# Kernel optimization log

Hardware: AMD Instinct MI355X
Metric: run time of the kernel (lower is better)

The kernel has to match this reference:

```python
import jax, jax.numpy as jnp
import numpy as np

E, D, H, K, DIL, T = 8, 768, 3072, 3, 1, 16384


def _conv1d(x, w, b, dilation):
    # x: [1, C_in, L]; w: [C_out, C_in, K]; torch Conv1d with SAME padding
    pad = dilation * (w.shape[-1] - 1) // 2
    y = jax.lax.conv_general_dilated(
        x, w, window_strides=(1,), padding=[(pad, pad)],
        rhs_dilation=(dilation,), dimension_numbers=("NCH", "OIH", "NCH"))
    return y + b[None, :, None]


def setup_inputs() -> dict:
    key = jax.random.key(0)
    k0, k1, k2, k3, k4 = jax.random.split(key, 5)
    inp = jax.random.normal(k0, (T, D), dtype=jnp.float32)
    fwd_expert_count = jnp.full((E,), T // E, dtype=jnp.int32)
    w1 = jax.random.normal(k1, (E, H, D, K), dtype=jnp.float32) * (1.0 / np.sqrt(D * K))
    b1 = jax.random.normal(k2, (E, H), dtype=jnp.float32) * 0.01
    w2 = jax.random.normal(k3, (E, D, H, K), dtype=jnp.float32) * (1.0 / np.sqrt(H * K))
    b2 = jax.random.normal(k4, (E, D), dtype=jnp.float32) * 0.01
    return {"inp": inp, "fwd_expert_count": fwd_expert_count,
            "w1": w1, "b1": b1, "w2": w2, "b2": b2}


def reference(inp, fwd_expert_count, w1, b1, w2, b2):
    # counts define static per-expert segment lengths (constants w.r.t. compute graph)
    counts = np.asarray(jax.device_get(fwd_expert_count))
    x = inp.T[None]  # [1, D, T]
    outs, idx = [], 0
    for i in range(counts.shape[0]):
        n = int(counts[i])
        if n > 0:
            outs.append(_conv1d(x[:, :, idx:idx + n], w1[i], b1[i], DIL))
            idx += n
    h = jax.nn.gelu(jnp.concatenate(outs, axis=2), approximate=False)  # [1, H, T]
    outs, idx = [], 0
    for i in range(counts.shape[0]):
        n = int(counts[i])
        if n > 0:
            outs.append(_conv1d(h[:, :, idx:idx + n], w2[i], b2[i], DIL))
            idx += n
    y = jnp.concatenate(outs, axis=2)[0]  # [D, T]
    return y.T  # [T, D]
```

## Files before the change

kernel.cpp:

```cpp
#include <hip/hip_runtime.h>
#include <hip/hip_bf16.h>
#include <cstdint>

#define E_   8
#define D_   768
#define H_   3072
#define T_   16384
#define SEG  2048
#define PSEG (SEG + 2)

typedef __attribute__((ext_vector_type(8))) __bf16 bf16x8;
typedef __attribute__((ext_vector_type(4))) float f32x4;
typedef __attribute__((ext_vector_type(4))) unsigned int u32x4;

__device__ inline unsigned short f2bf(float f) {
  union { float f; unsigned int u; } v; v.f = f;
  unsigned int u = v.u;
  u += 0x7fffu + ((u >> 16) & 1u);
  return (unsigned short)(u >> 16);
}

__device__ inline float gelu_exact(float x) {
  return 0.5f * x * (1.0f + erff(x * 0.70710678118654752f));
}

__device__ inline void gload16(const unsigned short* g, unsigned short* l) {
  __builtin_amdgcn_global_load_lds(
      (const __attribute__((address_space(1))) unsigned int*)g,
      (__attribute__((address_space(3))) unsigned int*)l, 16, 0, 0);
}

__global__ __launch_bounds__(256) void cvt_x_pad_kernel(const float* __restrict__ in,
                                                        unsigned short* __restrict__ out) {
  const int i = blockIdx.x * 256 + threadIdx.x;
  const int elem = i * 8;
  const int row = elem / D_;
  const int col = elem - row * D_;
  const int prow = (row >> 11) * PSEG + 1 + (row & (SEG - 1));
  const float* p = in + (size_t)row * D_ + col;
  u32x4 v;
#pragma unroll
  for (int j = 0; j < 4; ++j)
    v[j] = (unsigned)f2bf(p[2 * j]) | ((unsigned)f2bf(p[2 * j + 1]) << 16);
  *(u32x4*)(out + (size_t)prow * D_ + col) = v;
}

__global__ __launch_bounds__(256) void zero_guards_kernel(unsigned short* __restrict__ buf,
                                                          int C) {
  const int e = blockIdx.x >> 1;
  const size_t row = (size_t)e * PSEG + (blockIdx.x & 1) * (PSEG - 1);
  for (int c = threadIdx.x; c < C; c += 256) buf[row * C + c] = 0;
}

__global__ __launch_bounds__(256) void cvt_w_kernel(const float* __restrict__ in,
                                                    unsigned short* __restrict__ out,
                                                    int C) {
  int r = blockIdx.x;
  const float* src = in + (size_t)r * C * 3;
  unsigned short* dst = out + (size_t)r * C * 3;
  for (int c = threadIdx.x; c < C; c += 256) {
    float v0 = src[c * 3 + 0], v1 = src[c * 3 + 1], v2 = src[c * 3 + 2];
    dst[0 * C + c] = f2bf(v0);
    dst[1 * C + c] = f2bf(v1);
    dst[2 * C + c] = f2bf(v2);
  }
}

template <int CIN, int COUT, bool DO_GELU>
__global__ __launch_bounds__(512, 2) void conv_gemm8_kernel(
    const unsigned short* __restrict__ A,
    const unsigned short* __restrict__ Bt,
    const float* __restrict__ bias,
    void* __restrict__ Out) {
  __shared__ __align__(16) unsigned short lds[65536];

  constexpr int CSTEPS = CIN / 64;
  constexpr int NT = 3 * CSTEPS;
  constexpr int NTN = COUT / 256;

  const int tid  = threadIdx.x;
  const int wid  = tid >> 6, lane = tid & 63;
  const int wm   = wid >> 2, wn = wid & 3;

  const int bid = blockIdx.x;
  const int e   = bid & 7;
  const int rem = bid >> 3;
  const int mc  = rem / (4 * NTN);
  const int r2  = rem - mc * 4 * NTN;
  const int m0  = (mc * 4 + (r2 & 3)) * 256;
  const int n0  = (r2 >> 2) * 256;

  const int rowoff = tid >> 3;
  const int psrc   = ((lane & 7) ^ (lane >> 3)) * 8;
  const int ko     = (lane >> 4) * 16;
  const int ax     = (lane & 7) << 4;

  const size_t abase = ((size_t)e * PSEG + m0) * CIN;

  f32x4 acc[8][4];
#pragma unroll
  for (int n = 0; n < 4; ++n) {
    const float bv = bias[e * COUT + n0 + wn * 64 + n * 16 + (lane & 15)];
#pragma unroll
    for (int m = 0; m < 8; ++m) acc[m][n] = (f32x4){bv, bv, bv, bv};
  }

#define STAGE_A(kt_, part_) do {                                                     \
    const int ktu_ = (kt_);                                                          \
    const int ktc_ = ktu_ < NT ? ktu_ : NT - 1;    \
    const int k3_  = ktc_ / CSTEPS;                                                  \
    const int c0_  = (ktc_ - k3_ * CSTEPS) * 64;                                     \
    const int buf_ = ktu_ & 1;                                                       \
    _Pragma("unroll")                                                                \
    for (int ii_ = 0; ii_ < 2; ++ii_) {                                              \
      gload16(A + abase + (size_t)(ii_ * 128 + (part_) * 64 + rowoff + k3_) * CIN    \
                  + c0_ + psrc,                                                      \
              (unsigned short*)((char*)lds + buf_ * 32768 + ii_ * 16384 +            \
                                (part_) * 8192 + wid * 1024 + lane * 16));           \
    }                                                                                \
  } while (0)

#define STAGE_B(kt_, h_) do {                                                        \
    const int ktu_ = (kt_);                                                          \
    const int ktc_ = ktu_ < NT ? ktu_ : NT - 1;                                      \
    const int k3_  = ktc_ / CSTEPS;                                                  \
    const int c0_  = (ktc_ - k3_ * CSTEPS) * 64;                                     \
    const int buf_ = ktu_ & 1;                                                       \
    _Pragma("unroll")                                                                \
    for (int ii_ = 0; ii_ < 2; ++ii_) {                                              \
      const int brow_ = n0 + (h_) * 128 + ii_ * 64 + rowoff;                         \
      gload16(Bt + ((size_t)(e * COUT + brow_) * 3 + k3_) * CIN + c0_ + psrc,        \
              (unsigned short*)((char*)lds + 65536 + buf_ * 32768 + (h_) * 16384 +  \
                                ii_ * 8192 + wid * 1024 + lane * 16));               \
    }                                                                                \
  } while (0)

#define FULLBAR() do { asm volatile("" ::: "memory");                                \
                       __builtin_amdgcn_s_barrier();                                 \
                       asm volatile("" ::: "memory"); } while (0)
#define VM6() asm volatile("s_waitcnt vmcnt(6)" ::: "memory")

#define PHASE(cur_, j_, STAGE_STMT) do {                                             \
    bf16x8 aF[2][2];                                                                 \
    const char* Ab_ = (const char*)lds + (cur_) * 32768 + wm * 16384;                \
    if ((j_) == 0) {                                                                 \
      const char* Bb_ = (const char*)lds + 65536 + (cur_) * 32768 + (wn >> 1) * 16384; \
      _Pragma("unroll")                                                              \
      for (int n_ = 0; n_ < 4; ++n_)                                                 \
        _Pragma("unroll")                                                            \
        for (int s_ = 0; s_ < 2; ++s_)                                               \
          bF[n_][s_] = *(const bf16x8*)(Bb_ +                                        \
              ((wn & 1) * 64 + n_ * 16 + (lane & 15)) * 128 + ((s_ * 64 + ko) ^ ax)); \
    }                                                                                \
    _Pragma("unroll")                                                                \
    for (int mm_ = 0; mm_ < 2; ++mm_)                                                \
      _Pragma("unroll")                                                              \
      for (int s_ = 0; s_ < 2; ++s_)                                                 \
        aF[mm_][s_] = *(const bf16x8*)(Ab_ +                                         \
            (((j_) * 2 + mm_) * 16 + (lane & 15)) * 128 + ((s_ * 64 + ko) ^ ax));    \
    STAGE_STMT;                                                                      \
    FULLBAR();                                                                       \
    __builtin_amdgcn_s_setprio(1);                                                   \
    _Pragma("unroll")                                                                \
    for (int mm_ = 0; mm_ < 2; ++mm_)                                                \
      _Pragma("unroll")                                                              \
      for (int n_ = 0; n_ < 4; ++n_) {                                               \
        acc[(j_) * 2 + mm_][n_] = __builtin_amdgcn_mfma_f32_16x16x32_bf16(           \
            aF[mm_][0], bF[n_][0], acc[(j_) * 2 + mm_][n_], 0, 0, 0);                \
        acc[(j_) * 2 + mm_][n_] = __builtin_amdgcn_mfma_f32_16x16x32_bf16(           \
            aF[mm_][1], bF[n_][1], acc[(j_) * 2 + mm_][n_], 0, 0, 0);                \
      }                                                                              \
    __builtin_amdgcn_s_setprio(0);                                                   \
  } while (0)

  STAGE_B(0, 0); STAGE_B(0, 1); STAGE_A(0, 0); STAGE_A(0, 1);
  STAGE_B(1, 0); STAGE_B(1, 1); STAGE_A(1, 0);
  VM6();
  FULLBAR();

  bf16x8 bF[4][2];
  int kt0 = 0;
#pragma unroll 1
  for (int it = 0; it < NT / 2; ++it, kt0 += 2) {
    PHASE(0, 0, STAGE_A(kt0 + 1, 1));           FULLBAR();
    PHASE(0, 1, STAGE_B(kt0 + 2, 0));           FULLBAR();
    PHASE(0, 2, STAGE_B(kt0 + 2, 1));           FULLBAR();
    PHASE(0, 3, STAGE_A(kt0 + 2, 0));   VM6();  FULLBAR();
    PHASE(1, 0, STAGE_A(kt0 + 2, 1));           FULLBAR();
    PHASE(1, 1, STAGE_B(kt0 + 3, 0));           FULLBAR();
    PHASE(1, 2, STAGE_B(kt0 + 3, 1));           FULLBAR();
    PHASE(1, 3, STAGE_A(kt0 + 3, 0));   VM6();  FULLBAR();
  }

  asm volatile("s_waitcnt vmcnt(0)" ::: "memory");

#undef PHASE
#undef STAGE_A
#undef STAGE_B
#undef FULLBAR
#undef VM6

#pragma unroll
  for (int m = 0; m < 8; ++m) {
    const int rowb = m0 + wm * 128 + m * 16 + ((lane >> 4) << 2);
#pragma unroll
    for (int n = 0; n < 4; ++n) {
      const int col = n0 + wn * 64 + n * 16 + (lane & 15);
#pragma unroll
      for (int i = 0; i < 4; ++i) {
        if (DO_GELU) {
          const size_t off = ((size_t)e * PSEG + 1 + rowb + i) * COUT + col;
          ((unsigned short*)Out)[off] = f2bf(gelu_exact(acc[m][n][i]));
        } else {
          const size_t off = ((size_t)e * SEG + rowb + i) * COUT + col;
          ((float*)Out)[off] = acc[m][n][i];
        }
      }
    }
  }
}

extern "C" void kernel_launch(void* const* d_in, const int* in_sizes, int n_in,
                              void* d_out, int out_size, void* d_ws, size_t ws_size,
                              hipStream_t stream) {
  const float* inp = (const float*)d_in[0];
  const float* w1 = (const float*)d_in[2];
  const float* b1 = (const float*)d_in[3];
  const float* w2 = (const float*)d_in[4];
  const float* b2 = (const float*)d_in[5];
  float* out = (float*)d_out;
  char* ws = (char*)d_ws;

  const size_t szXp = (size_t)E_ * PSEG * D_ * 2;
  const size_t szHp = (size_t)E_ * PSEG * H_ * 2;
  const size_t szW1 = (size_t)E_ * H_ * 3 * D_ * 2;
  const size_t szW2 = (size_t)E_ * D_ * 3 * H_ * 2;

  unsigned short* Xp  = (unsigned short*)ws;
  unsigned short* Hp  = (unsigned short*)(ws + szXp);
  unsigned short* W1T = (unsigned short*)(ws + szXp + szHp);
  unsigned short* W2T = (unsigned short*)(ws + szXp + szHp + szW1);

  if (ws_size < szXp + szHp + szW1 + szW2) return;

  zero_guards_kernel<<<E_ * 2, 256, 0, stream>>>(Xp, D_);
  zero_guards_kernel<<<E_ * 2, 256, 0, stream>>>(Hp, H_);
  cvt_x_pad_kernel<<<T_ * D_ / 8 / 256, 256, 0, stream>>>(inp, Xp);
  cvt_w_kernel<<<E_ * H_, 256, 0, stream>>>(w1, W1T, D_);
  cvt_w_kernel<<<E_ * D_, 256, 0, stream>>>(w2, W2T, H_);

  constexpr int NWG1 = (H_ / 256) * (SEG / 256) * E_;
  constexpr int NWG2 = (D_ / 256) * (SEG / 256) * E_;
  conv_gemm8_kernel<D_, H_, true>
      <<<NWG1, 512, 0, stream>>>(Xp, W1T, b1, Hp);
  conv_gemm8_kernel<H_, D_, false>
      <<<NWG2, 512, 0, stream>>>(Hp, W2T, b2, out);
}
```

Measured before the change: 612.6 us.

## Restructure MFMA phase schedule by k-half and use fast sigmoid-form GELU

Reorganizes the double-buffered GEMM main loop so each phase covers four M sub-tiles for one K half, holding separate B fragment sets per half and reordering A/B global-to-LDS staging with adjusted vmcnt waits. The goal is fewer LDS fragment reloads and better overlap of loads with MFMA work. Separately, the exact erf GELU in the first conv's epilogue is replaced by a sigmoid-form approximation using hardware exp2 and reciprocal, cutting epilogue cost at the price of small numerical deviation from the exact GELU.

```diff
diff --git a/kernel.cpp b/kernel.cpp
--- a/kernel.cpp
+++ b/kernel.cpp
@@ -20,8 +20,12 @@
   return (unsigned short)(u >> 16);
 }
 
-__device__ inline float gelu_exact(float x) {
-  return 0.5f * x * (1.0f + erff(x * 0.70710678118654752f));
+__device__ inline float gelu_fast(float x) {
+  const float a = -2.302118131f;
+  const float b = -0.102944213f;
+  float z = x * __builtin_fmaf(b, x * x, a);
+  float e = __builtin_amdgcn_exp2f(z);
+  return x * __builtin_amdgcn_rcpf(1.0f + e);
 }
 
 __device__ inline void gload16(const unsigned short* g, unsigned short* l) {
@@ -139,57 +143,53 @@
                        __builtin_amdgcn_s_barrier();                                 \
                        asm volatile("" ::: "memory"); } while (0)
 #define VM6() asm volatile("s_waitcnt vmcnt(6)" ::: "memory")
-
-#define PHASE(cur_, j_, STAGE_STMT) do {                                             \
-    bf16x8 aF[2][2];                                                                 \
+#define VM8() asm volatile("s_waitcnt vmcnt(8)" ::: "memory")
+#define VM_NONE()
+
+#define PHASE(cur_, mq_, s_, RB_, bFa_, STAGE_STMT, VMW_) do {                       \
     const char* Ab_ = (const char*)lds + (cur_) * 32768 + wm * 16384;                \
-    if ((j_) == 0) {                                                                 \
+    if (RB_) {                                                                       \
       const char* Bb_ = (const char*)lds + 65536 + (cur_) * 32768 + (wn >> 1) * 16384; \
       _Pragma("unroll")                                                              \
       for (int n_ = 0; n_ < 4; ++n_)                                                 \
-        _Pragma("unroll")                                                            \
-        for (int s_ = 0; s_ < 2; ++s_)                                               \
-          bF[n_][s_] = *(const bf16x8*)(Bb_ +                                        \
-              ((wn & 1) * 64 + n_ * 16 + (lane & 15)) * 128 + ((s_ * 64 + ko) ^ ax)); \
+        bFa_[n_] = *(const bf16x8*)(Bb_ +                                            \
+            ((wn & 1) * 64 + n_ * 16 + (lane & 15)) * 128 + (((s_) * 64 + ko) ^ ax)); \
     }                                                                                \
-    _Pragma("unroll")                                                                \
-    for (int mm_ = 0; mm_ < 2; ++mm_)                                                \
-      _Pragma("unroll")                                                              \
-      for (int s_ = 0; s_ < 2; ++s_)                                                 \
-        aF[mm_][s_] = *(const bf16x8*)(Ab_ +                                         \
-            (((j_) * 2 + mm_) * 16 + (lane & 15)) * 128 + ((s_ * 64 + ko) ^ ax));    \
+    bf16x8 aF_[4];                                                                   \
+    _Pragma("unroll")                                                                \
+    for (int mi_ = 0; mi_ < 4; ++mi_)                                                \
+      aF_[mi_] = *(const bf16x8*)(Ab_ +                                              \
+          (((mq_) * 4 + mi_) * 16 + (lane & 15)) * 128 + (((s_) * 64 + ko) ^ ax));   \
     STAGE_STMT;                                                                      \
+    VMW_();                                                                          \
     FULLBAR();                                                                       \
     __builtin_amdgcn_s_setprio(1);                                                   \
     _Pragma("unroll")                                                                \
-    for (int mm_ = 0; mm_ < 2; ++mm_)                                                \
+    for (int mi_ = 0; mi_ < 4; ++mi_)                                                \
       _Pragma("unroll")                                                              \
-      for (int n_ = 0; n_ < 4; ++n_) {                                               \
-        acc[(j_) * 2 + mm_][n_] = __builtin_amdgcn_mfma_f32_16x16x32_bf16(           \
-            aF[mm_][0], bF[n_][0], acc[(j_) * 2 + mm_][n_], 0, 0, 0);                \
-        acc[(j_) * 2 + mm_][n_] = __builtin_amdgcn_mfma_f32_16x16x32_bf16(           \
-            aF[mm_][1], bF[n_][1], acc[(j_) * 2 + mm_][n_], 0, 0, 0);                \
-      }                                                                              \
+      for (int n_ = 0; n_ < 4; ++n_)                                                 \
+        acc[(mq_) * 4 + mi_][n_] = __builtin_amdgcn_mfma_f32_16x16x32_bf16(          \
+            aF_[mi_], bFa_[n_], acc[(mq_) * 4 + mi_][n_], 0, 0, 0);                  \
     __builtin_amdgcn_s_setprio(0);                                                   \
   } while (0)
 
   STAGE_B(0, 0); STAGE_B(0, 1); STAGE_A(0, 0); STAGE_A(0, 1);
-  STAGE_B(1, 0); STAGE_B(1, 1); STAGE_A(1, 0);
+  STAGE_B(1, 0); STAGE_B(1, 1);
   VM6();
   FULLBAR();
 
-  bf16x8 bF[4][2];
+  bf16x8 bF0[4], bF1[4];
   int kt0 = 0;
 #pragma unroll 1
   for (int it = 0; it < NT / 2; ++it, kt0 += 2) {
-    PHASE(0, 0, STAGE_A(kt0 + 1, 1));           FULLBAR();
-    PHASE(0, 1, STAGE_B(kt0 + 2, 0));           FULLBAR();
-    PHASE(0, 2, STAGE_B(kt0 + 2, 1));           FULLBAR();
-    PHASE(0, 3, STAGE_A(kt0 + 2, 0));   VM6();  FULLBAR();
-    PHASE(1, 0, STAGE_A(kt0 + 2, 1));           FULLBAR();
-    PHASE(1, 1, STAGE_B(kt0 + 3, 0));           FULLBAR();
-    PHASE(1, 2, STAGE_B(kt0 + 3, 1));           FULLBAR();
-    PHASE(1, 3, STAGE_A(kt0 + 3, 0));   VM6();  FULLBAR();
+    PHASE(0, 0, 0, 1, bF0, STAGE_A(kt0 + 1, 0), VM_NONE);  FULLBAR();
+    PHASE(0, 0, 1, 1, bF1, STAGE_A(kt0 + 1, 1), VM8);      FULLBAR();
+    PHASE(0, 1, 0, 0, bF0, STAGE_B(kt0 + 2, 0), VM_NONE);  FULLBAR();
+    PHASE(0, 1, 1, 0, bF1, STAGE_B(kt0 + 2, 1), VM6);      FULLBAR();
+    PHASE(1, 0, 0, 1, bF0, STAGE_A(kt0 + 2, 0), VM_NONE);  FULLBAR();
+    PHASE(1, 0, 1, 1, bF1, STAGE_A(kt0 + 2, 1), VM8);      FULLBAR();
+    PHASE(1, 1, 0, 0, bF0, STAGE_B(kt0 + 3, 0), VM_NONE);  FULLBAR();
+    PHASE(1, 1, 1, 0, bF1, STAGE_B(kt0 + 3, 1), VM6);      FULLBAR();
   }
 
   asm volatile("s_waitcnt vmcnt(0)" ::: "memory");
@@ -199,6 +199,8 @@
 #undef STAGE_B
 #undef FULLBAR
 #undef VM6
+#undef VM8
+#undef VM_NONE
 
 #pragma unroll
   for (int m = 0; m < 8; ++m) {
@@ -210,7 +212,7 @@
       for (int i = 0; i < 4; ++i) {
         if (DO_GELU) {
           const size_t off = ((size_t)e * PSEG + 1 + rowb + i) * COUT + col;
-          ((unsigned short*)Out)[off] = f2bf(gelu_exact(acc[m][n][i]));
+          ((unsigned short*)Out)[off] = f2bf(gelu_fast(acc[m][n][i]));
         } else {
           const size_t off = ((size_t)e * SEG + rowb + i) * COUT + col;
           ((float*)Out)[off] = acc[m][n][i];
```

Measured after the change: 572.8 us. 6.5% less time.
